# Kernel optimization log

Hardware: AMD Instinct MI355X
Metric: run time of the kernel (lower is better)

The kernel has to match this reference:

```python
import jax, jax.numpy as jnp
import numpy as np

N_HEAD = 8
HID = 64
IN_DIM = 512
OUT_DIM = 512


def setup_inputs() -> dict:
    key = jax.random.key(0)
    ks = jax.random.split(key, 12)
    B, LQ, LK = 2, 2048, 2048
    stdv = 1.0 / np.sqrt(HID)
    inp = {
        "q": jax.random.normal(ks[0], (B, LQ, IN_DIM), jnp.float32),
        "k": jax.random.normal(ks[1], (B, LK, IN_DIM), jnp.float32),
        "v": jax.random.normal(ks[2], (B, LK, IN_DIM), jnp.float32),
        # linear params stored as (in, out); torch Linear applies x @ W.T + b,
        # we store pre-transposed weights so y = x @ W + b is the same math.
        "Wq": jax.random.normal(ks[3], (IN_DIM, N_HEAD * HID), jnp.float32) * 0.02,
        "bq": jnp.zeros((N_HEAD * HID,), jnp.float32),
        "Wk": jax.random.normal(ks[4], (IN_DIM, N_HEAD * HID), jnp.float32) * 0.02,
        "bk": jnp.zeros((N_HEAD * HID,), jnp.float32),
        "Wv": jax.random.normal(ks[5], (IN_DIM, N_HEAD * HID), jnp.float32) * 0.02,
        "bv": jnp.zeros((N_HEAD * HID,), jnp.float32),
        # mlp-method scoring vector, uniform(-stdv, stdv), length 2*hidden
        "w_score": jax.random.uniform(ks[6], (2 * HID,), jnp.float32, -stdv, stdv),
        "Wd": jax.random.normal(ks[7], (N_HEAD * HID, OUT_DIM), jnp.float32) * 0.02,
        "bd": jnp.zeros((OUT_DIM,), jnp.float32),
    }
    return inp


def reference(q, k, v, Wq, bq, Wk, bk, Wv, bv, w_score, Wd, bd):
    B, Lq, _ = q.shape
    Lk = k.shape[1]
    # project and split heads -> (n_head, B, L, hid), matching torch's
    # permute(2,0,1,3).view(n_head*B, L, hid) layout
    qx = (q @ Wq + bq).reshape(B, Lq, N_HEAD, HID).transpose(2, 0, 1, 3)
    kx = (k @ Wk + bk).reshape(B, Lk, N_HEAD, HID).transpose(2, 0, 1, 3)
    vx = (v @ Wv + bv).reshape(B, Lk, N_HEAD, HID).transpose(2, 0, 1, 3)
    # 'mlp' additive attention: tanh(cat(q_i, k_j) . w) == tanh(q_i.w1 + k_j.w2)
    # computed as a broadcast sum instead of materializing the concat tensor
    w1, w2 = w_score[:HID], w_score[HID:]
    qw = qx @ w1  # (n_head, B, Lq)
    kw = kx @ w2  # (n_head, B, Lk)
    score = jnp.tanh(qw[..., :, None] + kw[..., None, :])  # (n_head, B, Lq, Lk)
    score = jax.nn.softmax(score, axis=-1)
    out_head = jnp.einsum('hbqk,hbkd->hbqd', score, vx)  # (n_head, B, Lq, hid)
    # torch: split along head*batch dim then cat along features -> head-major concat
    out = out_head.transpose(1, 2, 0, 3).reshape(B, Lq, N_HEAD * HID)
    output = out @ Wd + bd  # dropout is identity in eval
    score_flat = score.reshape(N_HEAD * B, Lq, Lk)
    return output, score_flat
```

## Files before the change

### kernel.cpp

```cpp
#include <hip/hip_runtime.h>
#include <math.h>

#define B_  2
#define L_  2048
#define D_  512
#define NH_ 8
#define HD_ 64

typedef __attribute__((ext_vector_type(8))) short short8;
typedef __attribute__((ext_vector_type(4))) float f32x4;

__device__ __forceinline__ float ex2(float x) {
#if __has_builtin(__builtin_amdgcn_exp2f)
    return __builtin_amdgcn_exp2f(x);
#else
    return exp2f(x);
#endif
}
__device__ __forceinline__ float rcp_(float x) {
#if __has_builtin(__builtin_amdgcn_rcpf)
    return __builtin_amdgcn_rcpf(x);
#else
    return 1.0f / x;
#endif
}

__device__ __forceinline__ float fast_e(float x) {
    float z  = ex2(x * 2.885390082f);
    float th = 1.0f - 2.0f * rcp_(z + 1.0f);
    return ex2(th * 1.4426950408889634f);
}

__device__ __forceinline__ unsigned int f2bf(float x) {
    unsigned int u = __float_as_uint(x);
    u += 0x7fffu + ((u >> 16) & 1u);
    return u >> 16;
}
__device__ __forceinline__ unsigned int pk2(float lo, float hi) {
    return f2bf(lo) | (f2bf(hi) << 16);
}

__global__ void k_prep(const float* __restrict__ Wq, const float* __restrict__ bq,
                       const float* __restrict__ Wk, const float* __restrict__ bk,
                       const float* __restrict__ wsc,
                       float* __restrict__ wqwT, float* __restrict__ wkwT,
                       float* __restrict__ bqw, float* __restrict__ bkw) {
    __shared__ float w[HD_];
    int which = blockIdx.x >> 1;
    int half  = blockIdx.x & 1;
    const float* W  = which ? Wk : Wq;
    const float* bb = which ? bk : bq;
    float* WT = which ? wkwT : wqwT;
    float* bo = which ? bkw  : bqw;
    if (threadIdx.x < HD_) w[threadIdx.x] = wsc[which * HD_ + threadIdx.x];
    __syncthreads();
    int r = half * 256 + threadIdx.x;
    for (int h = 0; h < NH_; ++h) {
        float s = 0.f;
        #pragma unroll 8
        for (int d = 0; d < HD_; ++d) s += W[r * D_ + h * HD_ + d] * w[d];
        WT[h * D_ + r] = s;
    }
    if (half == 0 && threadIdx.x < NH_) {
        int h = threadIdx.x;
        float s = 0.f;
        for (int d = 0; d < HD_; ++d) s += bb[h * HD_ + d] * w[d];
        bo[h] = s;
    }
}

__global__ void k_wconv(const float* __restrict__ Wv, const float* __restrict__ Wd,
                        unsigned short* __restrict__ WvF,
                        unsigned short* __restrict__ WdFh,
                        unsigned short* __restrict__ WdFl) {
    int id = blockIdx.x * 256 + threadIdx.x;
    int lane = id & 63;
    int kb = (id >> 6) & 15;
    int nf = id >> 10;
    int l15 = lane & 15, lg = lane >> 4;
    int n = nf * 16 + l15;
    int k0 = kb * 32 + lg * 4;
    size_t base = ((size_t)(nf * 16 + kb) * 64 + lane) * 8;
    if (blockIdx.y == 0) {
        #pragma unroll
        for (int j = 0; j < 8; ++j) {
            int k = k0 + (j & 3) + 16 * (j >> 2);
            WvF[base + j] = (unsigned short)f2bf(Wv[(size_t)k * 512 + n]);
        }
    } else {
        #pragma unroll
        for (int j = 0; j < 8; ++j) {
            int k = k0 + (j & 3) + 16 * (j >> 2);
            float x = Wd[(size_t)k * 512 + n];
            unsigned int h = f2bf(x);
            float hf = __uint_as_float(h << 16);
            WdFh[base + j] = (unsigned short)h;
            WdFl[base + j] = (unsigned short)f2bf(x - hf);
        }
    }
}

__global__ void k_qwkw(const float* __restrict__ q, const float* __restrict__ k,
                       const float* __restrict__ wqwT, const float* __restrict__ wkwT,
                       const float* __restrict__ bqw, const float* __restrict__ bkw,
                       float* __restrict__ qw, float* __restrict__ kw) {
    int wid  = blockIdx.x * 4 + (threadIdx.x >> 6);
    int lane = threadIdx.x & 63;
    int sel  = wid >= 4096;
    int row  = wid & 4095;
    const float* src = sel ? k : q;
    const float* WT  = sel ? wkwT : wqwT;
    const float* bo  = sel ? bkw : bqw;
    float* dst = sel ? kw : qw;
    float4 va = *(const float4*)(src + (size_t)row * D_ + lane * 4);
    float4 vb = *(const float4*)(src + (size_t)row * D_ + 256 + lane * 4);
    float res[NH_];
    #pragma unroll
    for (int h = 0; h < NH_; ++h) {
        float4 wa = *(const float4*)(WT + h * D_ + lane * 4);
        float4 wb = *(const float4*)(WT + h * D_ + 256 + lane * 4);
        float s = va.x*wa.x + va.y*wa.y + va.z*wa.z + va.w*wa.w
                + vb.x*wb.x + vb.y*wb.y + vb.z*wb.z + vb.w*wb.w;
        #pragma unroll
        for (int off = 32; off; off >>= 1) s += __shfl_xor(s, off);
        res[h] = s + bo[h];
    }
    if (lane == 0) {
        #pragma unroll
        for (int h = 0; h < NH_; ++h) dst[h * 4096 + row] = res[h];
    }
}

__global__ __launch_bounds__(256) void k_mmA(const float* __restrict__ A,
                                             const short8* __restrict__ BF,
                                             const float* __restrict__ bias,
                                             unsigned short* __restrict__ vxg) {
    int m0 = blockIdx.x * 64;
    int n0q = blockIdx.y * 4;
    int tid = threadIdx.x;
    int w = tid >> 6, lane = tid & 63;
    int l15 = lane & 15, lg = lane >> 4;
    f32x4 acc[4];
    #pragma unroll
    for (int j = 0; j < 4; ++j) acc[j] = (f32x4){0.f, 0.f, 0.f, 0.f};

    const float* a0 = A + (size_t)(m0 + w * 16 + l15) * 512 + lg * 4;

    float4 clo = *(const float4*)(a0);
    float4 chi = *(const float4*)(a0 + 16);
    short8 cb[4];
    #pragma unroll
    for (int nf = 0; nf < 4; ++nf) cb[nf] = BF[(size_t)(n0q + nf) * 16 * 64 + lane];

    for (int kb = 0; kb < 16; ++kb) {
        float4 lo = clo, hi = chi;
        short8 b0 = cb[0], b1 = cb[1], b2 = cb[2], b3 = cb[3];
        if (kb < 15) {
            clo = *(const float4*)(a0 + (kb + 1) * 32);
            chi = *(const float4*)(a0 + (kb + 1) * 32 + 16);
            #pragma unroll
            for (int nf = 0; nf < 4; ++nf)
                cb[nf] = BF[((size_t)(n0q + nf) * 16 + kb + 1) * 64 + lane];
        }
        union { unsigned int u[4]; short8 s; } af;
        af.u[0] = pk2(lo.x, lo.y); af.u[1] = pk2(lo.z, lo.w);
        af.u[2] = pk2(hi.x, hi.y); af.u[3] = pk2(hi.z, hi.w);
        acc[0] = __builtin_amdgcn_mfma_f32_16x16x32_bf16(af.s, b0, acc[0], 0, 0, 0);
        acc[1] = __builtin_amdgcn_mfma_f32_16x16x32_bf16(af.s, b1, acc[1], 0, 0, 0);
        acc[2] = __builtin_amdgcn_mfma_f32_16x16x32_bf16(af.s, b2, acc[2], 0, 0, 0);
        acc[3] = __builtin_amdgcn_mfma_f32_16x16x32_bf16(af.s, b3, acc[3], 0, 0, 0);
    }
    int m = m0 + w * 16 + lg * 4;
    int b = m >> 11, kk = m & 2047;
    int kblk = kk >> 5, base32 = kk & 31;
    int ie0 = 4 * (base32 >> 4);
    int lvsel = 16 * ((base32 >> 2) & 3);
    #pragma unroll
    for (int nf = 0; nf < 4; ++nf) {
        int n = (n0q + nf) * 16 + l15;
        float bvv = bias[n];
        int h = n >> 6, dt = (n >> 4) & 3, ncol = n & 15;
        int lane_v = ncol + lvsel;
        size_t ad = ((((size_t)((h * 2 + b) * 64 + kblk)) * 4 + dt) * 64 + lane_v) * 8 + ie0;
        uint2 pkt;
        pkt.x = pk2(acc[nf][0] + bvv, acc[nf][1] + bvv);
        pkt.y = pk2(acc[nf][2] + bvv, acc[nf][3] + bvv);
        *(uint2*)(vxg + ad) = pkt;
    }
}

__global__ __launch_bounds__(256) void k_mmB(const float* __restrict__ A,
                                             const short8* __restrict__ BFh,
                                             const short8* __restrict__ BFl,
                                             const float* __restrict__ bias,
                                             float* __restrict__ C) {
    int m0 = blockIdx.x * 64;
    int n0q = blockIdx.y * 4;
    int tid = threadIdx.x;
    int w = tid >> 6, lane = tid & 63;
    int l15 = lane & 15, lg = lane >> 4;
    f32x4 acc[4];
    #pragma unroll
    for (int j = 0; j < 4; ++j) acc[j] = (f32x4){0.f, 0.f, 0.f, 0.f};

    const float* a0 = A + (size_t)(m0 + w * 16 + l15) * 512 + lg * 4;

    float4 clo = *(const float4*)(a0);
    float4 chi = *(const float4*)(a0 + 16);

    for (int kb = 0; kb < 16; ++kb) {
        float4 lo = clo, hi = chi;
        if (kb < 15) {
            clo = *(const float4*)(a0 + (kb + 1) * 32);
            chi = *(const float4*)(a0 + (kb + 1) * 32 + 16);
        }
        union { unsigned int u[4]; short8 s; } ah, al;
        {
            float xs[8] = {lo.x, lo.y, lo.z, lo.w, hi.x, hi.y, hi.z, hi.w};
            unsigned int hu[8]; float lf[8];
            #pragma unroll
            for (int j = 0; j < 8; ++j) {
                hu[j] = f2bf(xs[j]);
                lf[j] = xs[j] - __uint_as_float(hu[j] << 16);
            }
            #pragma unroll
            for (int j = 0; j < 4; ++j) {
                ah.u[j] = hu[2 * j] | (hu[2 * j + 1] << 16);
                al.u[j] = pk2(lf[2 * j], lf[2 * j + 1]);
            }
        }
        #pragma unroll
        for (int nf = 0; nf < 4; ++nf) {
            size_t bi = ((size_t)(n0q + nf) * 16 + kb) * 64 + lane;
            short8 bh = BFh[bi];
            short8 bl = BFl[bi];
            acc[nf] = __builtin_amdgcn_mfma_f32_16x16x32_bf16(ah.s, bh, acc[nf], 0, 0, 0);
            acc[nf] = __builtin_amdgcn_mfma_f32_16x16x32_bf16(al.s, bh, acc[nf], 0, 0, 0);
            acc[nf] = __builtin_amdgcn_mfma_f32_16x16x32_bf16(ah.s, bl, acc[nf], 0, 0, 0);
        }
    }
    #pragma unroll
    for (int nf = 0; nf < 4; ++nf) {
        int n = (n0q + nf) * 16 + l15;
        float bdv = bias[n];
        #pragma unroll
        for (int r = 0; r < 4; ++r) {
            int m = m0 + w * 16 + lg * 4 + r;
            C[(size_t)m * 512 + n] = acc[nf][r] + bdv;
        }
    }
}

__global__ __launch_bounds__(512, 6) void k_main(const float* __restrict__ qw,
                                                 const float* __restrict__ kw,
                                                 const short8* __restrict__ vgs,
                                                 float* __restrict__ att,
                                                 float* __restrict__ rsum_o) {
    int hb  = blockIdx.x;
    int q0  = blockIdx.y * 64;
    int tid = threadIdx.x;
    int w   = tid >> 6;
    int wq  = w & 3;
    int kh  = w >> 2;
    int lane = tid & 63;
    int l15 = lane & 15, lg = lane >> 4;

    __shared__ float kws[2048];
    __shared__ float red[4][16][68];

    *(float4*)&kws[tid * 4] = *(const float4*)(kw + hb * 2048 + tid * 4);
    __syncthreads();

    float qwv = qw[hb * 2048 + q0 + wq * 16 + l15];
    const short8* bp = vgs + (size_t)hb * 16384 + lane;

    f32x4 acc0 = {0,0,0,0}, acc1 = {0,0,0,0}, acc2 = {0,0,0,0}, acc3 = {0,0,0,0};
    float sum = 0.f;

    int kb0 = kh * 32;
    const short8* pb = bp + (size_t)kb0 * 256;
    short8 cb0 = pb[0], cb1 = pb[64], cb2 = pb[128], cb3 = pb[192];

    for (int i = 0; i < 32; ++i) {
        short8 b0 = cb0, b1 = cb1, b2 = cb2, b3 = cb3;
        if (i < 31) {
            const short8* nb = bp + (size_t)(kb0 + i + 1) * 256;
            cb0 = nb[0]; cb1 = nb[64]; cb2 = nb[128]; cb3 = nb[192];
        }
        int kidx = (kb0 + i) * 32 + lg * 4;
        float4 kw0 = *(const float4*)&kws[kidx];
        float4 kw1 = *(const float4*)&kws[kidx + 16];
        float e0 = fast_e(qwv + kw0.x), e1 = fast_e(qwv + kw0.y);
        float e2 = fast_e(qwv + kw0.z), e3 = fast_e(qwv + kw0.w);
        float e4 = fast_e(qwv + kw1.x), e5 = fast_e(qwv + kw1.y);
        float e6 = fast_e(qwv + kw1.z), e7 = fast_e(qwv + kw1.w);
        sum += ((e0 + e1) + (e2 + e3)) + ((e4 + e5) + (e6 + e7));
        union { unsigned int u[4]; short8 s; } af;
        af.u[0] = pk2(e0, e1);
        af.u[1] = pk2(e2, e3);
        af.u[2] = pk2(e4, e5);
        af.u[3] = pk2(e6, e7);
        acc0 = __builtin_amdgcn_mfma_f32_16x16x32_bf16(af.s, b0, acc0, 0, 0, 0);
        acc1 = __builtin_amdgcn_mfma_f32_16x16x32_bf16(af.s, b1, acc1, 0, 0, 0);
        acc2 = __builtin_amdgcn_mfma_f32_16x16x32_bf16(af.s, b2, acc2, 0, 0, 0);
        acc3 = __builtin_amdgcn_mfma_f32_16x16x32_bf16(af.s, b3, acc3, 0, 0, 0);
    }

    sum += __shfl_xor(sum, 16);
    sum += __shfl_xor(sum, 32);

    if (kh == 1) {
        #define WR_(dt, accv) \
            red[wq][lg * 4 + 0][dt * 16 + l15] = accv[0]; \
            red[wq][lg * 4 + 1][dt * 16 + l15] = accv[1]; \
            red[wq][lg * 4 + 2][dt * 16 + l15] = accv[2]; \
            red[wq][lg * 4 + 3][dt * 16 + l15] = accv[3];
        WR_(0, acc0) WR_(1, acc1) WR_(2, acc2) WR_(3, acc3)
        #undef WR_
        if (lane < 16) red[wq][lane][64] = sum;
    }
    __syncthreads();
    if (kh == 0) {
        #define RD_(dt, accv) \
            accv[0] += red[wq][lg * 4 + 0][dt * 16 + l15]; \
            accv[1] += red[wq][lg * 4 + 1][dt * 16 + l15]; \
            accv[2] += red[wq][lg * 4 + 2][dt * 16 + l15]; \
            accv[3] += red[wq][lg * 4 + 3][dt * 16 + l15];
        RD_(0, acc0) RD_(1, acc1) RD_(2, acc2) RD_(3, acc3)
        #undef RD_
        float tot = sum + red[wq][l15][64];
        float rs = 1.0f / tot;
        if (lane < 16) rsum_o[hb * 2048 + q0 + wq * 16 + lane] = rs;

        int b_ = hb & 1, h = hb >> 1;
        float r0s = __shfl(rs, lg * 4 + 0);
        float r1s = __shfl(rs, lg * 4 + 1);
        float r2s = __shfl(rs, lg * 4 + 2);
        float r3s = __shfl(rs, lg * 4 + 3);
        float* ab = att + ((size_t)(b_ * 2048 + q0 + wq * 16 + lg * 4)) * 512 + h * 64 + l15;
        #define ST_(dt, accv) \
            ab[0 * 512 + dt * 16] = accv[0] * r0s; \
            ab[1 * 512 + dt * 16] = accv[1] * r1s; \
            ab[2 * 512 + dt * 16] = accv[2] * r2s; \
            ab[3 * 512 + dt * 16] = accv[3] * r3s;
        ST_(0, acc0) ST_(1, acc1) ST_(2, acc2) ST_(3, acc3)
        #undef ST_
    }
}

__global__ void k_score(const float* __restrict__ qw, const float* __restrict__ kw,
                        const float* __restrict__ rsum, float* __restrict__ score) {
    int hb = blockIdx.y;
    int tid = threadIdx.x;
    __shared__ float kws[2048];
    *(float4*)&kws[tid * 8]     = *(const float4*)(kw + hb * 2048 + tid * 8);
    *(float4*)&kws[tid * 8 + 4] = *(const float4*)(kw + hb * 2048 + tid * 8 + 4);
    __syncthreads();
    int rl  = tid >> 5;
    int t32 = tid & 31;
    int q = blockIdx.x * 8 + rl;
    float qwv = qw[hb * 2048 + q];
    float rs  = rsum[hb * 2048 + q];
    float* out = score + ((size_t)(hb * 2048 + q)) * 2048;
    #pragma unroll
    for (int i = 0; i < 16; ++i) {
        int k = i * 128 + t32 * 4;
        float4 o;
        o.x = fast_e(qwv + kws[k + 0]) * rs;
        o.y = fast_e(qwv + kws[k + 1]) * rs;
        o.z = fast_e(qwv + kws[k + 2]) * rs;
        o.w = fast_e(qwv + kws[k + 3]) * rs;
        *(float4*)(out + k) = o;
    }
}

extern "C" void kernel_launch(void* const* d_in, const int* in_sizes, int n_in,
                              void* d_out, int out_size, void* d_ws, size_t ws_size,
                              hipStream_t stream) {
    (void)in_sizes; (void)n_in; (void)out_size; (void)ws_size;
    const float* q   = (const float*)d_in[0];
    const float* k   = (const float*)d_in[1];
    const float* v   = (const float*)d_in[2];
    const float* Wq  = (const float*)d_in[3];
    const float* bq  = (const float*)d_in[4];
    const float* Wk  = (const float*)d_in[5];
    const float* bk  = (const float*)d_in[6];
    const float* Wv  = (const float*)d_in[7];
    const float* bv  = (const float*)d_in[8];
    const float* wsc = (const float*)d_in[9];
    const float* Wd  = (const float*)d_in[10];
    const float* bd  = (const float*)d_in[11];

    float* out   = (float*)d_out;
    float* score = out + (size_t)B_ * L_ * D_;

    float* ws    = (float*)d_ws;
    float* wqwT  = ws;
    float* wkwT  = ws + 4096;
    float* bqw   = ws + 8192;
    float* bkw   = ws + 8256;
    float* qw    = ws + 8704;
    float* kw    = ws + 41472;
    float* rsum  = ws + 74240;
    float* vxg   = ws + 107008;
    float* att   = ws + 1155584;
    float* WvF   = ws + 3252736;
    float* WdFh  = ws + 3383808;
    float* WdFl  = ws + 3514880;

    k_prep<<<dim3(4), dim3(256), 0, stream>>>(Wq, bq, Wk, bk, wsc, wqwT, wkwT, bqw, bkw);
    k_wconv<<<dim3(128, 2), dim3(256), 0, stream>>>(Wv, Wd,
        (unsigned short*)WvF, (unsigned short*)WdFh, (unsigned short*)WdFl);
    k_qwkw<<<dim3(2048), dim3(256), 0, stream>>>(q, k, wqwT, wkwT, bqw, bkw, qw, kw);
    k_mmA<<<dim3(64, 8), dim3(256), 0, stream>>>(v, (const short8*)WvF, bv,
        (unsigned short*)vxg);
    k_main<<<dim3(16, 32), dim3(512), 0, stream>>>(qw, kw, (const short8*)vxg, att, rsum);
    k_score<<<dim3(256, 16), dim3(256), 0, stream>>>(qw, kw, rsum, score);
    k_mmB<<<dim3(64, 8), dim3(256), 0, stream>>>(att, (const short8*)WdFh,
        (const short8*)WdFl, bd, out);
}
```

Before: 166.5 us.

## Compute softmax row sums via MFMA with ones and use hardware bf16 pack

```diff
diff --git a/kernel.cpp b/kernel.cpp
--- a/kernel.cpp
+++ b/kernel.cpp
@@ -163,8 +163,10 @@
                 cb[nf] = BF[((size_t)(n0q + nf) * 16 + kb + 1) * 64 + lane];
         }
         union { unsigned int u[4]; short8 s; } af;
-        af.u[0] = pk2(lo.x, lo.y); af.u[1] = pk2(lo.z, lo.w);
-        af.u[2] = pk2(hi.x, hi.y); af.u[3] = pk2(hi.z, hi.w);
+        asm("v_cvt_pk_bf16_f32 %0, %1, %2" : "=v"(af.u[0]) : "v"(lo.x), "v"(lo.y));
+        asm("v_cvt_pk_bf16_f32 %0, %1, %2" : "=v"(af.u[1]) : "v"(lo.z), "v"(lo.w));
+        asm("v_cvt_pk_bf16_f32 %0, %1, %2" : "=v"(af.u[2]) : "v"(hi.x), "v"(hi.y));
+        asm("v_cvt_pk_bf16_f32 %0, %1, %2" : "=v"(af.u[3]) : "v"(hi.z), "v"(hi.w));
         acc[0] = __builtin_amdgcn_mfma_f32_16x16x32_bf16(af.s, b0, acc[0], 0, 0, 0);
         acc[1] = __builtin_amdgcn_mfma_f32_16x16x32_bf16(af.s, b1, acc[1], 0, 0, 0);
         acc[2] = __builtin_amdgcn_mfma_f32_16x16x32_bf16(af.s, b2, acc[2], 0, 0, 0);
@@ -251,13 +253,13 @@
     }
 }
 
-__global__ __launch_bounds__(512, 6) void k_main(const float* __restrict__ qw,
+__global__ __launch_bounds__(512, 4) void k_main(const float* __restrict__ qw,
                                                  const float* __restrict__ kw,
                                                  const short8* __restrict__ vgs,
                                                  float* __restrict__ att,
                                                  float* __restrict__ rsum_o) {
-    int hb  = blockIdx.x;
-    int q0  = blockIdx.y * 64;
+    int hb  = blockIdx.y;
+    int q0  = blockIdx.x * 64;
     int tid = threadIdx.x;
     int w   = tid >> 6;
     int wq  = w & 3;
@@ -275,39 +277,42 @@
     const short8* bp = vgs + (size_t)hb * 16384 + lane;
 
     f32x4 acc0 = {0,0,0,0}, acc1 = {0,0,0,0}, acc2 = {0,0,0,0}, acc3 = {0,0,0,0};
-    float sum = 0.f;
+    f32x4 accs = {0,0,0,0};
+    union { unsigned int u[4]; short8 s; } ones_;
+    ones_.u[0] = 0x3f803f80u; ones_.u[1] = 0x3f803f80u;
+    ones_.u[2] = 0x3f803f80u; ones_.u[3] = 0x3f803f80u;
 
     int kb0 = kh * 32;
     const short8* pb = bp + (size_t)kb0 * 256;
     short8 cb0 = pb[0], cb1 = pb[64], cb2 = pb[128], cb3 = pb[192];
+    float4 ckw0 = *(const float4*)&kws[kb0 * 32 + lg * 4];
+    float4 ckw1 = *(const float4*)&kws[kb0 * 32 + lg * 4 + 16];
 
     for (int i = 0; i < 32; ++i) {
         short8 b0 = cb0, b1 = cb1, b2 = cb2, b3 = cb3;
+        float4 kw0 = ckw0, kw1 = ckw1;
         if (i < 31) {
             const short8* nb = bp + (size_t)(kb0 + i + 1) * 256;
             cb0 = nb[0]; cb1 = nb[64]; cb2 = nb[128]; cb3 = nb[192];
-        }
-        int kidx = (kb0 + i) * 32 + lg * 4;
-        float4 kw0 = *(const float4*)&kws[kidx];
-        float4 kw1 = *(const float4*)&kws[kidx + 16];
+            int nk = (kb0 + i + 1) * 32 + lg * 4;
+            ckw0 = *(const float4*)&kws[nk];
+            ckw1 = *(const float4*)&kws[nk + 16];
+        }
         float e0 = fast_e(qwv + kw0.x), e1 = fast_e(qwv + kw0.y);
         float e2 = fast_e(qwv + kw0.z), e3 = fast_e(qwv + kw0.w);
         float e4 = fast_e(qwv + kw1.x), e5 = fast_e(qwv + kw1.y);
         float e6 = fast_e(qwv + kw1.z), e7 = fast_e(qwv + kw1.w);
-        sum += ((e0 + e1) + (e2 + e3)) + ((e4 + e5) + (e6 + e7));
         union { unsigned int u[4]; short8 s; } af;
-        af.u[0] = pk2(e0, e1);
-        af.u[1] = pk2(e2, e3);
-        af.u[2] = pk2(e4, e5);
-        af.u[3] = pk2(e6, e7);
+        asm("v_cvt_pk_bf16_f32 %0, %1, %2" : "=v"(af.u[0]) : "v"(e0), "v"(e1));
+        asm("v_cvt_pk_bf16_f32 %0, %1, %2" : "=v"(af.u[1]) : "v"(e2), "v"(e3));
+        asm("v_cvt_pk_bf16_f32 %0, %1, %2" : "=v"(af.u[2]) : "v"(e4), "v"(e5));
+        asm("v_cvt_pk_bf16_f32 %0, %1, %2" : "=v"(af.u[3]) : "v"(e6), "v"(e7));
         acc0 = __builtin_amdgcn_mfma_f32_16x16x32_bf16(af.s, b0, acc0, 0, 0, 0);
         acc1 = __builtin_amdgcn_mfma_f32_16x16x32_bf16(af.s, b1, acc1, 0, 0, 0);
         acc2 = __builtin_amdgcn_mfma_f32_16x16x32_bf16(af.s, b2, acc2, 0, 0, 0);
         acc3 = __builtin_amdgcn_mfma_f32_16x16x32_bf16(af.s, b3, acc3, 0, 0, 0);
-    }
-
-    sum += __shfl_xor(sum, 16);
-    sum += __shfl_xor(sum, 32);
+        accs = __builtin_amdgcn_mfma_f32_16x16x32_bf16(af.s, ones_.s, accs, 0, 0, 0);
+    }
 
     if (kh == 1) {
         #define WR_(dt, accv) \
@@ -317,7 +322,12 @@
             red[wq][lg * 4 + 3][dt * 16 + l15] = accv[3];
         WR_(0, acc0) WR_(1, acc1) WR_(2, acc2) WR_(3, acc3)
         #undef WR_
-        if (lane < 16) red[wq][lane][64] = sum;
+        if (l15 == 0) {
+            red[wq][lg * 4 + 0][64] = accs[0];
+            red[wq][lg * 4 + 1][64] = accs[1];
+            red[wq][lg * 4 + 2][64] = accs[2];
+            red[wq][lg * 4 + 3][64] = accs[3];
+        }
     }
     __syncthreads();
     if (kh == 0) {
@@ -328,21 +338,23 @@
             accv[3] += red[wq][lg * 4 + 3][dt * 16 + l15];
         RD_(0, acc0) RD_(1, acc1) RD_(2, acc2) RD_(3, acc3)
         #undef RD_
-        float tot = sum + red[wq][l15][64];
-        float rs = 1.0f / tot;
-        if (lane < 16) rsum_o[hb * 2048 + q0 + wq * 16 + lane] = rs;
-
+        float rs0 = 1.0f / (accs[0] + red[wq][lg * 4 + 0][64]);
+        float rs1 = 1.0f / (accs[1] + red[wq][lg * 4 + 1][64]);
+        float rs2 = 1.0f / (accs[2] + red[wq][lg * 4 + 2][64]);
+        float rs3 = 1.0f / (accs[3] + red[wq][lg * 4 + 3][64]);
+        if (l15 == 0) {
+            rsum_o[hb * 2048 + q0 + wq * 16 + lg * 4 + 0] = rs0;
+            rsum_o[hb * 2048 + q0 + wq * 16 + lg * 4 + 1] = rs1;
+            rsum_o[hb * 2048 + q0 + wq * 16 + lg * 4 + 2] = rs2;
+            rsum_o[hb * 2048 + q0 + wq * 16 + lg * 4 + 3] = rs3;
+        }
         int b_ = hb & 1, h = hb >> 1;
-        float r0s = __shfl(rs, lg * 4 + 0);
-        float r1s = __shfl(rs, lg * 4 + 1);
-        float r2s = __shfl(rs, lg * 4 + 2);
-        float r3s = __shfl(rs, lg * 4 + 3);
         float* ab = att + ((size_t)(b_ * 2048 + q0 + wq * 16 + lg * 4)) * 512 + h * 64 + l15;
         #define ST_(dt, accv) \
-            ab[0 * 512 + dt * 16] = accv[0] * r0s; \
-            ab[1 * 512 + dt * 16] = accv[1] * r1s; \
-            ab[2 * 512 + dt * 16] = accv[2] * r2s; \
-            ab[3 * 512 + dt * 16] = accv[3] * r3s;
+            ab[0 * 512 + dt * 16] = accv[0] * rs0; \
+            ab[1 * 512 + dt * 16] = accv[1] * rs1; \
+            ab[2 * 512 + dt * 16] = accv[2] * rs2; \
+            ab[3 * 512 + dt * 16] = accv[3] * rs3;
         ST_(0, acc0) ST_(1, acc1) ST_(2, acc2) ST_(3, acc3)
         #undef ST_
     }
@@ -414,7 +426,7 @@
     k_qwkw<<<dim3(2048), dim3(256), 0, stream>>>(q, k, wqwT, wkwT, bqw, bkw, qw, kw);
     k_mmA<<<dim3(64, 8), dim3(256), 0, stream>>>(v, (const short8*)WvF, bv,
         (unsigned short*)vxg);
-    k_main<<<dim3(16, 32), dim3(512), 0, stream>>>(qw, kw, (const short8*)vxg, att, rsum);
+    k_main<<<dim3(32, 16), dim3(512), 0, stream>>>(qw, kw, (const short8*)vxg, att, rsum);
     k_score<<<dim3(256, 16), dim3(256), 0, stream>>>(qw, kw, rsum, score);
     k_mmB<<<dim3(64, 8), dim3(256), 0, stream>>>(att, (const short8*)WdFh,
         (const short8*)WdFl, bd, out);
```

New measurement: 160.1 us. -3.8%, faster.
